# Kernel optimization log

Hardware: AMD Instinct MI355X
Metric: run time of the kernel (lower is better)

## Reference

```python
import jax, jax.numpy as jnp
import numpy as np

B, S, H, T = 64, 512, 768, 9


def setup_inputs() -> dict:
    key = jax.random.key(0)
    ks = jax.random.split(key, 8)
    embeddings = jax.random.normal(ks[0], (B, S, H), dtype=jnp.float32)
    # variable-length mask (first token always valid), as token_type_ids would give
    lengths = jax.random.randint(ks[1], (B,), 1, S + 1)
    mask = (jnp.arange(S)[None, :] < lengths[:, None]).astype(jnp.int32)
    labels = jax.random.randint(ks[2], (B, S), 0, T)
    W = jax.random.normal(ks[3], (T, H), dtype=jnp.float32) * (1.0 / np.sqrt(H))
    b = jnp.zeros((T,), dtype=jnp.float32)
    start_trans = jax.random.normal(ks[4], (T,), dtype=jnp.float32) * 0.1
    transitions = jax.random.normal(ks[5], (T, T), dtype=jnp.float32) * 0.1
    end_trans = jax.random.normal(ks[6], (T,), dtype=jnp.float32) * 0.1
    return {"embeddings": embeddings, "W": W, "b": b,
            "start_trans": start_trans, "transitions": transitions,
            "end_trans": end_trans, "labels": labels, "mask": mask}


def _crf_nll(emissions, labels, mask_bool, start_trans, transitions, end_trans):
    # emissions: [B,S,T]; returns negative log-likelihood per sequence [B]
    Bn = emissions.shape[0]
    mask_f = mask_bool.astype(emissions.dtype)
    # --- gold path score (numerator) ---
    first = start_trans[labels[:, 0]] + emissions[jnp.arange(Bn), 0, labels[:, 0]]
    emis_sc = jnp.take_along_axis(emissions, labels[..., None], axis=2)[..., 0]  # [B,S]
    trans_sc = transitions[labels[:, :-1], labels[:, 1:]]                         # [B,S-1]
    num = first + jnp.sum((emis_sc[:, 1:] + trans_sc) * mask_f[:, 1:], axis=1)
    last_idx = jnp.sum(mask_bool.astype(jnp.int32), axis=1) - 1
    last_lab = jnp.take_along_axis(labels, last_idx[:, None], axis=1)[:, 0]
    num = num + end_trans[last_lab]
    # --- log partition (forward algorithm, logsumexp recurrence) ---
    alpha0 = start_trans[None, :] + emissions[:, 0]          # [B,T]
    em_t = jnp.swapaxes(emissions, 0, 1)[1:]                 # [S-1,B,T]
    m_t = mask_bool.T[1:]                                    # [S-1,B]
    def step(alpha, xs):
        em, m = xs
        new = jax.nn.logsumexp(alpha[:, :, None] + transitions[None], axis=1) + em
        return jnp.where(m[:, None], new, alpha), None
    alpha, _ = jax.lax.scan(step, alpha0, (em_t, m_t))
    denom = jax.nn.logsumexp(alpha + end_trans[None, :], axis=1)
    return denom - num


def reference(embeddings, W, b, start_trans, transitions, end_trans, labels, mask):
    # dropout is identity at eval; Linear + ReLU emissions
    emissions = jax.nn.relu(jnp.einsum('bsh,th->bst', embeddings, W) + b)
    # -100 padding handling: zero out mask there, clamp labels to 0
    valid = labels != -100
    mask_bool = (mask != 0) & valid
    labels_mod = jnp.where(valid, labels, 0)
    nll = _crf_nll(emissions, labels_mod, mask_bool, start_trans, transitions, end_trans)
    return jnp.mean(nll)  # == -loss.mean() of the log-likelihood
```

## Files before the change

### kernel.cpp

```cpp
#include <hip/hip_runtime.h>

#define NEG_INF (-1e30f)

static constexpr int Bn = 64;
static constexpr int Sn = 512;
static constexpr int Hn = 768;
static constexpr int Tn = 9;
static constexpr int KC = 32;
static constexpr int PSTRIDE = 108;
static constexpr int TPAD = 20;

__device__ __forceinline__ float dot4(float4 a, float4 b) {
    return a.x * b.x + a.y * b.y + a.z * b.z + a.w * b.w;
}

__global__ __launch_bounds__(512, 4) void fused_kernel(
        const float* __restrict__ emb, const float* __restrict__ Wm,
        const float* __restrict__ bias, const float* __restrict__ trans,
        const int* __restrict__ labels, const int* __restrict__ mask,
        float* __restrict__ chunkP, float* __restrict__ auxN,
        int* __restrict__ auxC, float* __restrict__ emRow0) {
    const int blk  = blockIdx.x;
    const int tid  = threadIdx.x;
    const int lane = tid & 63;
    const int seg  = __builtin_amdgcn_readfirstlane(tid >> 6);

    __shared__ float tileU[8][64 * TPAD];
    __shared__ float em_s[64][10];
    __shared__ float tr_s[81];

    const int rowBase = blk * 64;
    const float4* eg = (const float4*)emb;

    float4 stg[4];
#pragma unroll
    for (int j = 0; j < 4; ++j) {
        int z = j * 64 + lane, r = z >> 2, c4 = z & 3;
        stg[j] = eg[(size_t)(rowBase + r) * 192 + seg * 24 + c4];
    }
    if (tid < 81) tr_s[tid] = trans[tid];

    float* tile = &tileU[seg][0];
#pragma unroll
    for (int j = 0; j < 4; ++j) {
        int z = j * 64 + lane, r = z >> 2, c4 = z & 3;
        *(float4*)&tile[r * TPAD + c4 * 4] = stg[j];
    }

    float acc[Tn];
#pragma unroll
    for (int t = 0; t < Tn; ++t) acc[t] = 0.0f;

#pragma unroll
    for (int sb = 0; sb < 6; ++sb) {
        float4 nst[4];
        if (sb < 5) {
#pragma unroll
            for (int j = 0; j < 4; ++j) {
                int z = j * 64 + lane, r = z >> 2, c4 = z & 3;
                nst[j] = eg[(size_t)(rowBase + r) * 192 + seg * 24 + (sb + 1) * 4 + c4];
            }
        }
#pragma unroll
        for (int c4 = 0; c4 < 4; ++c4) {
            float4 e = *(const float4*)&tile[lane * TPAD + c4 * 4];
#pragma unroll
            for (int t = 0; t < Tn; ++t) {
                const float* wp = Wm + t * Hn + seg * 96 + sb * 16 + c4 * 4;
                float4 wv = *(const float4*)wp;
                acc[t] += dot4(e, wv);
            }
        }
        if (sb < 5) {
#pragma unroll
            for (int j = 0; j < 4; ++j) {
                int z = j * 64 + lane, r = z >> 2, c4 = z & 3;
                *(float4*)&tile[r * TPAD + c4 * 4] = nst[j];
            }
        }
    }

#pragma unroll
    for (int t = 0; t < Tn; ++t) tileU[seg][lane * Tn + t] = acc[t];
    __syncthreads();

    for (int o = tid; o < 64 * Tn; o += 512) {
        int r = o / Tn, t = o - r * Tn;
        float s = 0.0f;
#pragma unroll
        for (int sg = 0; sg < 8; ++sg) s += tileU[sg][o];
        float v = fmaxf(s + bias[t], 0.0f);
        em_s[r][t] = v;
        if ((blk & 7) == 0 && r == 0) emRow0[(blk >> 3) * Tn + t] = v;
    }
    __syncthreads();

    const int w  = tid >> 6;
    const int h  = w & 1;
    const int cl = w >> 1;
    const int b  = blk >> 3;
    const int sc = (blk & 7) * 4 + cl;
    const int s0 = (blk & 7) * 64;

    const int u16 = lane & 15;
    const int tstep = s0 + cl * 16 + u16;
    int lb = 0, on = 0;
    if (lane < 16) {
        lb = labels[b * Sn + tstep];
        int mm = mask[b * Sn + tstep];
        on = (tstep >= 1) && (mm != 0) && (lb != -100);
    }
    unsigned long long bm = __ballot(on != 0);

    if (h == 0) {
        float np = 0.0f;
        int c1 = 0;
        if (lane < 16 && on) {
            int lpr = labels[b * Sn + tstep - 1];
            lpr = (lpr == -100) ? 0 : lpr;
            np = em_s[cl * 16 + u16][lb] + tr_s[lpr * Tn + lb];
            c1 = 1;
        }
#pragma unroll
        for (int off = 8; off; off >>= 1) {
            np += __shfl_xor(np, off);
            c1 += __shfl_xor(c1, off);
        }
        if (lane == 0) { auxN[b * KC + sc] = np; auxC[b * KC + sc] = c1; }
    }

    const int v  = lane / 9;
    const int jj = lane - v * 9;
    const bool act = lane < (h ? 36 : 45);
    const int rid = h ? (5 + v) : v;

    float c[Tn];
#pragma unroll
    for (int kk = 0; kk < Tn; ++kk) c[kk] = tr_s[kk * Tn + jj];

    float pv = (act && rid == jj) ? 0.0f : NEG_INF;

    for (int u = 0; u < 16; ++u) {
        if (!((bm >> u) & 1ull)) continue;
        float x[Tn];
#pragma unroll
        for (int kk = 0; kk < Tn; ++kk) {
            float a = __shfl(pv, (v * Tn + kk) & 63);
            x[kk] = a + c[kk];
        }
        float mx = x[0];
#pragma unroll
        for (int kk = 1; kk < Tn; ++kk) mx = fmaxf(mx, x[kk]);
        float s = 0.0f;
#pragma unroll
        for (int kk = 0; kk < Tn; ++kk) s += __expf(x[kk] - mx);
        float nv = mx + __logf(s) + em_s[cl * 16 + u][jj];
        pv = act ? nv : pv;
    }
    if (act) chunkP[(size_t)(b * KC + sc) * PSTRIDE + jj * 12 + rid] = pv;
}

__global__ __launch_bounds__(64) void combine_kernel(
        const float* __restrict__ emRow0, const float* __restrict__ startT,
        const float* __restrict__ endT, const int* __restrict__ labels,
        const int* __restrict__ mask, const float* __restrict__ chunkP,
        const float* __restrict__ auxN, const int* __restrict__ auxC,
        float* __restrict__ nll) {
    const int b = blockIdx.x;
    const int lane = threadIdx.x;

    float em0 = (lane < Tn) ? emRow0[b * Tn + lane] : NEG_INF;
    float alpha = (lane < Tn) ? (startT[lane] + em0) : NEG_INF;

    int lab0r = labels[b * Sn];
    int lab0 = (lab0r == -100) ? 0 : lab0r;
    float first = startT[lab0] + __shfl(em0, lab0);

    float numP = (lane < KC) ? auxN[b * KC + lane] : 0.0f;
    int   cntP = (lane < KC) ? auxC[b * KC + lane] : 0;
#pragma unroll
    for (int off = 32; off; off >>= 1) {
        numP += __shfl_xor(numP, off);
        cntP += __shfl_xor(cntP, off);
    }
    int m0 = ((mask[b * Sn] != 0) && (lab0r != -100)) ? 1 : 0;
    int cntTot = cntP + m0;
    int lastIdx = cntTot - 1;
    if (lastIdx < 0) lastIdx = 0;
    int lastLab = labels[b * Sn + lastIdx];
    lastLab = (lastLab == -100) ? 0 : lastLab;
    float num = first + numP + endT[lastLab];

    const float* Pb = chunkP + (size_t)b * KC * PSTRIDE;
    float4 p0 = make_float4(0, 0, 0, 0), p1 = p0, p2 = p0;
    if (lane < Tn) {
        const float4* pp = (const float4*)(Pb + lane * 12);
        p0 = pp[0]; p1 = pp[1]; p2 = pp[2];
    }
    for (int k = 0; k < KC; ++k) {
        float4 q0 = p0, q1 = p1, q2 = p2;
        if (k + 1 < KC && lane < Tn) {
            const float4* pp = (const float4*)(Pb + (size_t)(k + 1) * PSTRIDE + lane * 12);
            p0 = pp[0]; p1 = pp[1]; p2 = pp[2];
        }
        float av[Tn];
#pragma unroll
        for (int i = 0; i < Tn; ++i) av[i] = __shfl(alpha, i);
        float x[Tn];
        x[0] = av[0] + q0.x; x[1] = av[1] + q0.y; x[2] = av[2] + q0.z;
        x[3] = av[3] + q0.w; x[4] = av[4] + q1.x; x[5] = av[5] + q1.y;
        x[6] = av[6] + q1.z; x[7] = av[7] + q1.w; x[8] = av[8] + q2.x;
        float mx = x[0];
#pragma unroll
        for (int i = 1; i < Tn; ++i) mx = fmaxf(mx, x[i]);
        float s = 0.0f;
#pragma unroll
        for (int i = 0; i < Tn; ++i) s += __expf(x[i] - mx);
        float na = mx + __logf(s);
        alpha = (lane < Tn) ? na : NEG_INF;
    }

    float z = (lane < Tn) ? (alpha + endT[lane]) : NEG_INF;
    float mx = z;
#pragma unroll
    for (int off = 32; off; off >>= 1) mx = fmaxf(mx, __shfl_xor(mx, off));
    float s = __expf(z - mx);
#pragma unroll
    for (int off = 32; off; off >>= 1) s += __shfl_xor(s, off);
    float denom = mx + __logf(s);

    if (lane == 0) nll[b] = denom - num;
}

__global__ __launch_bounds__(64) void mean_kernel(const float* __restrict__ nll,
        float* __restrict__ out) {
    float v = nll[threadIdx.x];
#pragma unroll
    for (int off = 32; off; off >>= 1) v += __shfl_xor(v, off);
    if (threadIdx.x == 0) out[0] = v * (1.0f / 64.0f);
}

extern "C" void kernel_launch(void* const* d_in, const int* in_sizes, int n_in,
                              void* d_out, int out_size, void* d_ws, size_t ws_size,
                              hipStream_t stream) {
    const float* emb    = (const float*)d_in[0];
    const float* Wm     = (const float*)d_in[1];
    const float* bias   = (const float*)d_in[2];
    const float* startT = (const float*)d_in[3];
    const float* trans  = (const float*)d_in[4];
    const float* endT   = (const float*)d_in[5];
    const int*   labels = (const int*)d_in[6];
    const int*   mask   = (const int*)d_in[7];

    float* chunkP = (float*)d_ws;
    float* auxN   = chunkP + (size_t)Bn * KC * PSTRIDE;
    int*   auxC   = (int*)(auxN + (size_t)Bn * KC);
    float* nll    = (float*)(auxC + (size_t)Bn * KC);
    float* emRow0 = nll + Bn;
    float* out    = (float*)d_out;

    fused_kernel<<<512, 512, 0, stream>>>(emb, Wm, bias, trans, labels, mask,
                                          chunkP, auxN, auxC, emRow0);
    combine_kernel<<<Bn, 64, 0, stream>>>(emRow0, startT, endT, labels, mask,
                                          chunkP, auxN, auxC, nll);
    mean_kernel<<<1, 64, 0, stream>>>(nll, out);
}
```

Measured before the change: 62.01 us.

## Compute emissions projection with bf16 MFMA instead of scalar FP32 dot products

Replaces the per-lane FP32 dot-product projection, which staged embeddings through shared memory, with 16x16x32 bf16 MFMA instructions. Each wave handles one 16-row tile over half of the hidden dimension, holding W fragments in registers and prefetching A rows straight from global memory. The two K-halves are then summed through a small shared buffer. The shared-memory staging goes away and matrix cores are used, but inputs are rounded to bf16, which lowers the precision of the emissions.

Measured after the change: 55.93 us. 1.11x faster.

```diff
diff --git a/kernel.cpp b/kernel.cpp
--- a/kernel.cpp
+++ b/kernel.cpp
@@ -8,10 +8,20 @@
 static constexpr int Tn = 9;
 static constexpr int KC = 32;
 static constexpr int PSTRIDE = 108;
-static constexpr int TPAD = 20;
-
-__device__ __forceinline__ float dot4(float4 a, float4 b) {
-    return a.x * b.x + a.y * b.y + a.z * b.z + a.w * b.w;
+
+typedef __attribute__((ext_vector_type(8))) short short8;
+typedef __attribute__((ext_vector_type(4))) float f32x4;
+
+__device__ __forceinline__ short f2bf(float x) {
+    __bf16 h = (__bf16)x;
+    return __builtin_bit_cast(short, h);
+}
+
+__device__ __forceinline__ short8 pack_bf16x8(float4 a, float4 b) {
+    short8 r;
+    r[0] = f2bf(a.x); r[1] = f2bf(a.y); r[2] = f2bf(a.z); r[3] = f2bf(a.w);
+    r[4] = f2bf(b.x); r[5] = f2bf(b.y); r[6] = f2bf(b.z); r[7] = f2bf(b.w);
+    return r;
 }
 
 __global__ __launch_bounds__(512, 4) void fused_kernel(
@@ -23,81 +33,74 @@
     const int blk  = blockIdx.x;
     const int tid  = threadIdx.x;
     const int lane = tid & 63;
-    const int seg  = __builtin_amdgcn_readfirstlane(tid >> 6);
-
-    __shared__ float tileU[8][64 * TPAD];
+    const int wv   = tid >> 6;
+    const int tile = wv & 3;
+    const int kh   = wv >> 2;
+
+    __shared__ float emH[2][64][10];
     __shared__ float em_s[64][10];
     __shared__ float tr_s[81];
 
+    if (tid < 81) tr_s[tid] = trans[tid];
+
+    const int t9 = lane & 15;
+    const int kg = lane >> 4;
+
+    short8 wf[12];
+    {
+        const float* wrow = Wm + t9 * Hn + kh * 384 + kg * 8;
+#pragma unroll
+        for (int s = 0; s < 12; ++s) {
+            if (t9 < Tn) {
+                float4 w0 = *(const float4*)(wrow + s * 32);
+                float4 w1 = *(const float4*)(wrow + s * 32 + 4);
+                wf[s] = pack_bf16x8(w0, w1);
+            } else {
+                short8 z = {0, 0, 0, 0, 0, 0, 0, 0};
+                wf[s] = z;
+            }
+        }
+    }
+
     const int rowBase = blk * 64;
-    const float4* eg = (const float4*)emb;
-
-    float4 stg[4];
-#pragma unroll
-    for (int j = 0; j < 4; ++j) {
-        int z = j * 64 + lane, r = z >> 2, c4 = z & 3;
-        stg[j] = eg[(size_t)(rowBase + r) * 192 + seg * 24 + c4];
-    }
-    if (tid < 81) tr_s[tid] = trans[tid];
-
-    float* tile = &tileU[seg][0];
-#pragma unroll
-    for (int j = 0; j < 4; ++j) {
-        int z = j * 64 + lane, r = z >> 2, c4 = z & 3;
-        *(float4*)&tile[r * TPAD + c4 * 4] = stg[j];
-    }
-
-    float acc[Tn];
-#pragma unroll
-    for (int t = 0; t < Tn; ++t) acc[t] = 0.0f;
-
-#pragma unroll
-    for (int sb = 0; sb < 6; ++sb) {
-        float4 nst[4];
-        if (sb < 5) {
-#pragma unroll
-            for (int j = 0; j < 4; ++j) {
-                int z = j * 64 + lane, r = z >> 2, c4 = z & 3;
-                nst[j] = eg[(size_t)(rowBase + r) * 192 + seg * 24 + (sb + 1) * 4 + c4];
-            }
-        }
-#pragma unroll
-        for (int c4 = 0; c4 < 4; ++c4) {
-            float4 e = *(const float4*)&tile[lane * TPAD + c4 * 4];
-#pragma unroll
-            for (int t = 0; t < Tn; ++t) {
-                const float* wp = Wm + t * Hn + seg * 96 + sb * 16 + c4 * 4;
-                float4 wv = *(const float4*)wp;
-                acc[t] += dot4(e, wv);
-            }
-        }
-        if (sb < 5) {
-#pragma unroll
-            for (int j = 0; j < 4; ++j) {
-                int z = j * 64 + lane, r = z >> 2, c4 = z & 3;
-                *(float4*)&tile[r * TPAD + c4 * 4] = nst[j];
-            }
-        }
-    }
-
-#pragma unroll
-    for (int t = 0; t < Tn; ++t) tileU[seg][lane * Tn + t] = acc[t];
+    const float* arow = emb + (size_t)(rowBase + tile * 16 + t9) * Hn
+                        + kh * 384 + kg * 8;
+    float4 pf0[4], pf1[4];
+#pragma unroll
+    for (int d = 0; d < 4; ++d) {
+        pf0[d] = *(const float4*)(arow + d * 32);
+        pf1[d] = *(const float4*)(arow + d * 32 + 4);
+    }
+    f32x4 acc = {0.0f, 0.0f, 0.0f, 0.0f};
+#pragma unroll
+    for (int s = 0; s < 12; ++s) {
+        float4 a0 = pf0[s & 3];
+        float4 a1 = pf1[s & 3];
+        if (s + 4 < 12) {
+            pf0[s & 3] = *(const float4*)(arow + (s + 4) * 32);
+            pf1[s & 3] = *(const float4*)(arow + (s + 4) * 32 + 4);
+        }
+        short8 af = pack_bf16x8(a0, a1);
+        acc = __builtin_amdgcn_mfma_f32_16x16x32_bf16(af, wf[s], acc, 0, 0, 0);
+    }
+
+    if (t9 < Tn) {
+#pragma unroll
+        for (int r = 0; r < 4; ++r)
+            emH[kh][tile * 16 + kg * 4 + r][t9] = acc[r];
+    }
     __syncthreads();
 
     for (int o = tid; o < 64 * Tn; o += 512) {
         int r = o / Tn, t = o - r * Tn;
-        float s = 0.0f;
-#pragma unroll
-        for (int sg = 0; sg < 8; ++sg) s += tileU[sg][o];
-        float v = fmaxf(s + bias[t], 0.0f);
+        float v = fmaxf(emH[0][r][t] + emH[1][r][t] + bias[t], 0.0f);
         em_s[r][t] = v;
         if ((blk & 7) == 0 && r == 0) emRow0[(blk >> 3) * Tn + t] = v;
     }
     __syncthreads();
 
-    const int w  = tid >> 6;
-    const int h  = w & 1;
-    const int cl = w >> 1;
+    const int h  = wv & 1;
+    const int cl = wv >> 1;
     const int b  = blk >> 3;
     const int sc = (blk & 7) * 4 + cl;
     const int s0 = (blk & 7) * 64;
```
